# Performance work log

Hardware: AMD Instinct MI355X
Metric: run time of the kernel (lower is better)

The kernel has to match this reference:

```python
import jax, jax.numpy as jnp
import numpy as np

B_, H_, W_ = 4, 64, 64
D_MODEL, D_INNER, N_STATE, R_RANK, K_ = 96, 192, 16, 6, 4
EPS = 1e-5

def silu(v):
    return v * jax.nn.sigmoid(v)

def setup_inputs() -> dict:
    key = jax.random.key(0)
    ks = jax.random.split(key, 8)
    d, dm = D_INNER, D_MODEL
    A = jnp.tile(jnp.arange(1, N_STATE + 1, dtype=jnp.float32)[None, :], (K_ * d, 1))
    return {
        "x": jax.random.normal(ks[0], (B_, H_, W_, dm), jnp.float32),
        "in_proj_w": jax.random.normal(ks[1], (2 * d, dm), jnp.float32) * 0.02,
        "conv_w": jax.random.normal(ks[2], (d, 1, 3, 3), jnp.float32) * 0.1,
        "conv_b": jnp.zeros((d,), jnp.float32),
        "x_proj_weight": jax.random.normal(ks[3], (K_, R_RANK + 2 * N_STATE, d), jnp.float32) * 0.05,
        "dt_projs_weight": jax.random.normal(ks[4], (K_, d, R_RANK), jnp.float32) * 0.1,
        "dt_projs_bias": jax.random.normal(ks[5], (K_, d), jnp.float32) * 0.1,
        "A_logs": jnp.log(A),
        "Ds": jnp.ones((K_ * d,), jnp.float32),
        "out_norm_w": jnp.ones((d,), jnp.float32),
        "out_norm_b": jnp.zeros((d,), jnp.float32),
        "out_proj_w": jax.random.normal(ks[6], (dm, d), jnp.float32) * 0.02,
    }

def selective_scan(u, dts, As, Bs, Cs, Ds, dt_bias):
    # u, dts: [B,K,D,L]; As: [K,D,N]; Bs, Cs: [B,K,N,L]; Ds, dt_bias: [K,D]
    delta = jax.nn.softplus(dts + dt_bias[None, :, :, None])
    dT = jnp.moveaxis(delta, -1, 0)  # [L,B,K,D]
    uT = jnp.moveaxis(u, -1, 0)      # [L,B,K,D]
    BT = jnp.moveaxis(Bs, -1, 0)     # [L,B,K,N]
    CT = jnp.moveaxis(Cs, -1, 0)     # [L,B,K,N]
    h0 = jnp.zeros((u.shape[0], K_, D_INNER, N_STATE), jnp.float32)

    def step(h, inps):
        dt, ut, bt, ct = inps
        h = jnp.exp(dt[..., None] * As[None]) * h + (dt * ut)[..., None] * bt[:, :, None, :]
        y = jnp.einsum('bkdn,bkn->bkd', h, ct)
        return h, y

    _, ys = jax.lax.scan(step, h0, (dT, uT, BT, CT))
    ys = jnp.moveaxis(ys, 0, -1)  # [B,K,D,L]
    return ys + u * Ds[None, :, :, None]

def reference(x, in_proj_w, conv_w, conv_b, x_proj_weight, dt_projs_weight,
              dt_projs_bias, A_logs, Ds, out_norm_w, out_norm_b, out_proj_w):
    B, H, W, dm = x.shape
    d, N, R, K = D_INNER, N_STATE, R_RANK, K_
    L = H * W
    # in_proj + z gate (SiLU)
    xz = jnp.einsum('bhwc,pc->bhwp', x, in_proj_w)  # [B,H,W,2d]
    xc, z = xz[..., :d], xz[..., d:]
    z = silu(z)
    # depthwise conv (NCHW) + SiLU
    xc = jnp.transpose(xc, (0, 3, 1, 2))  # [B,d,H,W]
    xc = jax.lax.conv_general_dilated(
        xc, conv_w, (1, 1), 'SAME', feature_group_count=d,
        dimension_numbers=('NCHW', 'OIHW', 'NCHW')) + conv_b[None, :, None, None]
    xc = silu(xc)
    # cross-scan: 4 directions
    x0 = xc.reshape(B, d, L)                                   # row-major
    x1 = jnp.transpose(xc, (0, 1, 3, 2)).reshape(B, d, L)       # col-major
    xs = jnp.stack([x0, x1, x0[..., ::-1], x1[..., ::-1]], axis=1)  # [B,K,D,L]
    # projections
    x_dbl = jnp.einsum('bkdl,kcd->bkcl', xs, x_proj_weight)
    dts, Bs, Cs = jnp.split(x_dbl, [R, R + N], axis=2)
    dts = jnp.einsum('bkrl,kdr->bkdl', dts, dt_projs_weight)
    As = -jnp.exp(A_logs).reshape(K, d, N)
    ys = selective_scan(xs, dts, As, Bs, Cs, Ds.reshape(K, d), dt_projs_bias)
    # cross-merge
    y_wh = (ys[:, 1] + ys[:, 3, :, ::-1]).reshape(B, d, W, H)
    y_wh = jnp.transpose(y_wh, (0, 1, 3, 2)).reshape(B, d, L)
    y = ys[:, 0] + ys[:, 2, :, ::-1] + y_wh                     # [B,d,L]
    y = jnp.transpose(y.reshape(B, d, H, W), (0, 2, 3, 1))       # [B,H,W,d]
    # out_norm: LayerNorm over channel dim
    mu = jnp.mean(y, axis=-1, keepdims=True)
    var = jnp.mean((y - mu) ** 2, axis=-1, keepdims=True)
    y = out_norm_w * (y - mu) * jax.lax.rsqrt(var + EPS) + out_norm_b
    # gate + out_proj
    y = y * z
    return jnp.einsum('bhwd,cd->bhwc', y, out_proj_w)
```

## Files before the change

kernel.cpp:

```cpp
#include <hip/hip_runtime.h>
#include <math.h>

#define B_ 4
#define HH 64
#define WW 64
#define LL 4096
#define DM 96
#define DI 192
#define NS 16
#define RR 6
#define KK 4
#define NROW (B_ * KK * DI)
#define XPS 160
#define KOFF 40

__device__ __forceinline__ int pix_of(int k, int l) {
    switch (k) {
        case 0: return l;
        case 1: { int w = l >> 6, h = l & 63; return (h << 6) + w; }
        case 2: return (LL - 1) - l;
        default: { int ll = (LL - 1) - l; int w = ll >> 6, h = ll & 63; return (h << 6) + w; }
    }
}

__device__ __forceinline__ float silu_f(float v) {
    return v * __fdividef(1.f, 1.f + __expf(-v));
}
__device__ __forceinline__ float softplus_f(float x) {
    return (x > 20.f) ? x : __logf(1.f + __expf(x));
}

template<int MODE>
__global__ __launch_bounds__(256)
void gemm_kernel(const float* __restrict__ A, const float* __restrict__ Bw,
                 float* __restrict__ C0, float* __restrict__ C1,
                 int M, int N, int Kd) {
    __shared__ float As[32][68];
    __shared__ float Bs[32][68];
    int tid = threadIdx.x;
    int tx = tid & 15, ty = tid >> 4;
    int m0 = blockIdx.y * 64, n0 = blockIdx.x * 64;
    float acc[4][4] = {};
    for (int k0 = 0; k0 < Kd; k0 += 32) {
        #pragma unroll
        for (int i = 0; i < 8; ++i) {
            int idx = tid + i * 256;
            int r = idx >> 5, c = idx & 31;
            As[c][r] = A[(size_t)(m0 + r) * Kd + k0 + c];
            int rn = n0 + r;
            Bs[c][r] = (rn < N) ? Bw[(size_t)rn * Kd + k0 + c] : 0.f;
        }
        __syncthreads();
        #pragma unroll
        for (int kk = 0; kk < 32; ++kk) {
            float4 av = *(const float4*)&As[kk][ty * 4];
            float4 bv = *(const float4*)&Bs[kk][tx * 4];
            const float* avp = (const float*)&av;
            const float* bvp = (const float*)&bv;
            #pragma unroll
            for (int i = 0; i < 4; ++i)
                #pragma unroll
                for (int j = 0; j < 4; ++j)
                    acc[i][j] += avp[i] * bvp[j];
        }
        __syncthreads();
    }
    #pragma unroll
    for (int i = 0; i < 4; ++i) {
        int m = m0 + ty * 4 + i;
        #pragma unroll
        for (int j = 0; j < 4; ++j) {
            int n = n0 + tx * 4 + j;
            if (n >= N) continue;
            float v = acc[i][j];
            if (MODE == 0) {
                if (n < DI) C0[(size_t)m * DI + n] = v;
                else        C1[(size_t)m * DI + (n - DI)] = silu_f(v);
            } else if (MODE == 1) {
                C0[(size_t)m * N + n] = v;
            } else {
                if (n < 152) {
                    int kd = n / 38, c = n - kd * 38;
                    C0[(size_t)m * XPS + kd * KOFF + c] = v;
                }
            }
        }
    }
}

__global__ __launch_bounds__(192)
void conv_kernel(const float* __restrict__ xc, const float* __restrict__ cw,
                 const float* __restrict__ cb, float* __restrict__ out) {
    int p0 = blockIdx.x * 8;
    int b = blockIdx.y;
    int c = threadIdx.x;
    int h = p0 >> 6, w0 = p0 & 63;
    float kw[9];
    #pragma unroll
    for (int j = 0; j < 9; ++j) kw[j] = cw[c * 9 + j];
    float xv[3][10];
    #pragma unroll
    for (int dh = 0; dh < 3; ++dh) {
        int hh = h + dh - 1;
        bool hv = (hh >= 0 && hh < HH);
        #pragma unroll
        for (int j = 0; j < 10; ++j) {
            int ww = w0 + j - 1;
            bool v = hv && (ww >= 0 && ww < WW);
            xv[dh][j] = v ? xc[((size_t)(b << 12) + (hh << 6) + ww) * DI + c] : 0.f;
        }
    }
    float bias = cb[c];
    #pragma unroll
    for (int w = 0; w < 8; ++w) {
        float acc = bias;
        #pragma unroll
        for (int dh = 0; dh < 3; ++dh)
            #pragma unroll
            for (int dc = 0; dc < 3; ++dc)
                acc += xv[dh][w + dc] * kw[dh * 3 + dc];
        out[((size_t)(b << 12) + p0 + w) * DI + c] = silu_f(acc);
    }
}

__global__ __launch_bounds__(256)
void prep_kernel(const float* __restrict__ A_logs, int* __restrict__ flag) {
    int t = blockIdx.x * 256 + threadIdx.x;
    if (t >= KK * DI * NS) return;
    int n = t & 15;
    float an = -__expf(A_logs[t]);
    if (!(fabsf(an + (float)(n + 1)) < 1e-4f * (float)(n + 1))) atomicOr(flag, 1);
}

template<int PHASE, int NCHT>
__global__ __launch_bounds__(192)
void scan_phase(const float* __restrict__ xconv, const float* __restrict__ xdblP,
                const float* __restrict__ dtw, const float* __restrict__ dtb,
                const float* __restrict__ A_logs, const float* __restrict__ Ds,
                float* __restrict__ sumD, float* __restrict__ carryB,
                float* __restrict__ y_acc, const int* __restrict__ flag) {
    constexpr int CHL = LL / NCHT;
    constexpr int NV4 = (PHASE == 3) ? (KOFF / 4) : 6;
    int chunk = blockIdx.x;
    int k = blockIdx.y;
    int b = blockIdx.z;
    int d = threadIdx.x;
    int l0 = chunk * CHL;
    __shared__ float sx[CHL * NV4 * 4];
    float4* sx4 = (float4*)sx;
    const float* xb = xdblP + ((size_t)(b << 12)) * XPS + k * KOFF;
    for (int idx = d; idx < CHL * NV4; idx += DI) {
        int r = idx / NV4, j = idx - r * NV4;
        int p = pix_of(k, l0 + r);
        sx4[idx] = *(const float4*)(xb + (size_t)p * XPS + j * 4);
    }

    float wr[RR];
    #pragma unroll
    for (int r = 0; r < RR; ++r) wr[r] = dtw[(k * DI + d) * RR + r];
    float bias = dtb[k * DI + d];
    const float* alog = A_logs + (size_t)(k * DI + d) * NS;
    bool fastA = (*flag == 0);
    float h[NS];
    int row = (b * KK + k) * DI + d;
    if (PHASE == 1) {
        #pragma unroll
        for (int n = 0; n < NS; ++n) h[n] = 0.f;
    } else {
        const float4* cb4 = (const float4*)(carryB + ((size_t)chunk * NROW + row) * NS);
        #pragma unroll
        for (int q = 0; q < NS / 4; ++q) {
            float4 v = cb4[q];
            h[q * 4 + 0] = v.x; h[q * 4 + 1] = v.y;
            h[q * 4 + 2] = v.z; h[q * 4 + 3] = v.w;
        }
    }
    float Dk = (PHASE == 3) ? Ds[k * DI + d] : 0.f;
    float sumDelta = 0.f;
    __syncthreads();

    int s = (k == 0) ? 1 : (k == 1) ? 64 : (k == 2) ? -1 : -64;
    int p0 = pix_of(k, l0);
    intptr_t stp = (intptr_t)s * DI;
    const float* up = xconv + (size_t)(b << 12) * DI + (size_t)p0 * DI + d;
    float* yp = y_acc + (size_t)(b << 12) * DI + (size_t)p0 * DI + d;
    float u_cur = *up;

    for (int i = 0; i < CHL; ++i) {
        float u_nxt = 0.f;
        if (i + 1 < CHL) u_nxt = up[stp];
        float xrv[NV4 * 4];
        float4* x4 = (float4*)xrv;
        #pragma unroll
        for (int j = 0; j < NV4; ++j) x4[j] = sx4[i * NV4 + j];
        float dtraw = bias;
        #pragma unroll
        for (int r = 0; r < RR; ++r) dtraw += xrv[r] * wr[r];
        float delta = softplus_f(dtraw);
        if (PHASE == 1) sumDelta += delta;
        float du = delta * u_cur;
        float y = 0.f;
        if (fastA) {
            float g = __expf(-delta);
            float a = 1.f;
            #pragma unroll
            for (int n = 0; n < NS; ++n) {
                a *= g;
                h[n] = a * h[n] + du * xrv[6 + n];
                if (PHASE == 3) y += h[n] * xrv[22 + n];
            }
        } else {
            #pragma unroll
            for (int n = 0; n < NS; ++n) {
                float a = __expf(delta * (-__expf(alog[n])));
                h[n] = a * h[n] + du * xrv[6 + n];
                if (PHASE == 3) y += h[n] * xrv[22 + n];
            }
        }
        if (PHASE == 3) {
            y += u_cur * Dk;
            atomicAdd(yp, y);
            yp += stp;
        }
        up += stp;
        u_cur = u_nxt;
    }
    if (PHASE == 1) {
        float4* cb4 = (float4*)(carryB + ((size_t)chunk * NROW + row) * NS);
        #pragma unroll
        for (int q = 0; q < NS / 4; ++q) {
            float4 vb;
            vb.x = h[q * 4 + 0]; vb.y = h[q * 4 + 1];
            vb.z = h[q * 4 + 2]; vb.w = h[q * 4 + 3];
            cb4[q] = vb;
        }
        sumD[(size_t)chunk * NROW + row] = sumDelta;
    }
}

template<int NCHT>
__global__ __launch_bounds__(256)
void scan_chunks(const float* __restrict__ sumD, const float* __restrict__ A_logs,
                 float* __restrict__ carryB) {
    int t = blockIdx.x * 256 + threadIdx.x;
    if (t >= NROW * NS) return;
    int row = t >> 4, n = t & 15;
    int kd = row % (KK * DI);
    float An = -__expf(A_logs[(size_t)kd * NS + n]);
    float h = 0.f;
    for (int c = 0; c < NCHT; ++c) {
        size_t idx = (size_t)c * (NROW * NS) + t;
        float bb = carryB[idx];
        carryB[idx] = h;
        float a = __expf(An * sumD[(size_t)c * NROW + row]);
        h = a * h + bb;
    }
}

__global__ __launch_bounds__(256)
void ln_kernel(const float* __restrict__ y_acc, const float* __restrict__ z_silu,
               const float* __restrict__ nw, const float* __restrict__ nb,
               float* __restrict__ out) {
    int pg = blockIdx.x * 4 + (threadIdx.x >> 6);
    int lane = threadIdx.x & 63;
    const float* yr = y_acc + (size_t)pg * DI;
    float v0 = yr[lane], v1 = yr[lane + 64], v2 = yr[lane + 128];
    float s = v0 + v1 + v2;
    float sq = v0 * v0 + v1 * v1 + v2 * v2;
    #pragma unroll
    for (int m = 32; m >= 1; m >>= 1) {
        s  += __shfl_xor(s, m, 64);
        sq += __shfl_xor(sq, m, 64);
    }
    float mu = s * (1.f / 192.f);
    float var = sq * (1.f / 192.f) - mu * mu;
    float rs = rsqrtf(var + 1e-5f);
    const float* zr = z_silu + (size_t)pg * DI;
    float* o = out + (size_t)pg * DI;
    float vv[3] = {v0, v1, v2};
    #pragma unroll
    for (int j = 0; j < 3; ++j) {
        int c = lane + j * 64;
        o[c] = (nw[c] * (vv[j] - mu) * rs + nb[c]) * zr[c];
    }
}

extern "C" void kernel_launch(void* const* d_in, const int* in_sizes, int n_in,
                              void* d_out, int out_size, void* d_ws, size_t ws_size,
                              hipStream_t stream) {
    const float* x        = (const float*)d_in[0];
    const float* in_projw = (const float*)d_in[1];
    const float* conv_w   = (const float*)d_in[2];
    const float* conv_b   = (const float*)d_in[3];
    const float* x_projw  = (const float*)d_in[4];
    const float* dt_w     = (const float*)d_in[5];
    const float* dt_b     = (const float*)d_in[6];
    const float* A_logs   = (const float*)d_in[7];
    const float* Ds       = (const float*)d_in[8];
    const float* nw       = (const float*)d_in[9];
    const float* nb       = (const float*)d_in[10];
    const float* opw      = (const float*)d_in[11];
    float* out = (float*)d_out;
    float* ws = (float*)d_ws;

    const size_t SZ = (size_t)B_ * LL * DI;
    const size_t XD = (size_t)B_ * LL * XPS;
    const size_t CAR256 = (size_t)NROW * 256 * NS;
    const size_t CAR128 = (size_t)NROW * 128 * NS;
    const size_t need256 = (3 * SZ + XD + CAR256 + (size_t)NROW * 256 + 16) * sizeof(float);
    bool big = (ws_size >= need256);

    float* z_silu = ws;
    float* xc_raw = ws + SZ;
    float* xconv  = ws + 2 * SZ;
    float* xdblP  = ws + 3 * SZ;
    float* carryB = ws + 3 * SZ + XD;
    float* sumD   = carryB + (big ? CAR256 : CAR128);
    int*   flag   = (int*)(sumD + (size_t)NROW * (big ? 256 : 128));
    float* y_acc  = xc_raw;
    float* yln    = xconv;

    gemm_kernel<0><<<dim3(6, 256), 256, 0, stream>>>(x, in_projw, xc_raw, z_silu,
                                                     B_ * LL, 2 * DI, DM);
    hipMemsetAsync(flag, 0, sizeof(int), stream);
    prep_kernel<<<(KK * DI * NS + 255) / 256, 256, 0, stream>>>(A_logs, flag);
    conv_kernel<<<dim3(LL / 8, B_), DI, 0, stream>>>(xc_raw, conv_w, conv_b, xconv);
    gemm_kernel<2><<<dim3(3, 256), 256, 0, stream>>>(xconv, x_projw, xdblP, nullptr,
                                                     B_ * LL, 152, DI);

    if (big) {
        scan_phase<1, 256><<<dim3(256, KK, B_), DI, 0, stream>>>(xconv, xdblP, dt_w, dt_b,
                                                                 A_logs, Ds, sumD, carryB, nullptr, flag);
        scan_chunks<256><<<(NROW * NS + 255) / 256, 256, 0, stream>>>(sumD, A_logs, carryB);
        hipMemsetAsync(y_acc, 0, SZ * sizeof(float), stream);
        scan_phase<3, 256><<<dim3(256, KK, B_), DI, 0, stream>>>(xconv, xdblP, dt_w, dt_b,
                                                                 A_logs, Ds, sumD, carryB, y_acc, flag);
    } else {
        scan_phase<1, 128><<<dim3(128, KK, B_), DI, 0, stream>>>(xconv, xdblP, dt_w, dt_b,
                                                                 A_logs, Ds, sumD, carryB, nullptr, flag);
        scan_chunks<128><<<(NROW * NS + 255) / 256, 256, 0, stream>>>(sumD, A_logs, carryB);
        hipMemsetAsync(y_acc, 0, SZ * sizeof(float), stream);
        scan_phase<3, 128><<<dim3(128, KK, B_), DI, 0, stream>>>(xconv, xdblP, dt_w, dt_b,
                                                                 A_logs, Ds, sumD, carryB, y_acc, flag);
    }
    ln_kernel<<<(B_ * LL) / 4, 256, 0, stream>>>(y_acc, z_silu, nw, nb, yln);
    gemm_kernel<1><<<dim3(2, 256), 256, 0, stream>>>(yln, opw, out, nullptr,
                                                     B_ * LL, DM, DI);
}
```

Measured before the change: 235.0 us.

## Pair forward/reverse scan directions per block and drop atomic y accumulation

Each scan block now processes a direction and its reversed counterpart (k and k+2) over mirrored chunks, so both touch the same pixels. Outputs go into a shared-memory accumulator and are written once with plain stores. Results land in two buffers (row-pair and column-pair) that the LayerNorm kernel sums, which removes the global atomics and the y memset. The cost is an extra workspace buffer and two sequential phase-3 launches with fewer blocks each. The xdbl rows are now read straight from global memory instead of being staged in LDS.

Measured after the change: 257.6 us. 9.6% more time.

```diff
diff --git a/kernel.cpp b/kernel.cpp
--- a/kernel.cpp
+++ b/kernel.cpp
@@ -134,71 +134,72 @@
 
 template<int PHASE, int NCHT>
 __global__ __launch_bounds__(192)
-void scan_phase(const float* __restrict__ xconv, const float* __restrict__ xdblP,
-                const float* __restrict__ dtw, const float* __restrict__ dtb,
-                const float* __restrict__ A_logs, const float* __restrict__ Ds,
-                float* __restrict__ sumD, float* __restrict__ carryB,
-                float* __restrict__ y_acc, const int* __restrict__ flag) {
+void scan_paired(const float* __restrict__ xconv, const float* __restrict__ xdblP,
+                 const float* __restrict__ dtw, const float* __restrict__ dtb,
+                 const float* __restrict__ A_logs, const float* __restrict__ Ds,
+                 float* __restrict__ sumD, float* __restrict__ carryB,
+                 float* __restrict__ yout, const int* __restrict__ flag, int pairArg) {
     constexpr int CHL = LL / NCHT;
     constexpr int NV4 = (PHASE == 3) ? (KOFF / 4) : 6;
-    int chunk = blockIdx.x;
-    int k = blockIdx.y;
+    int c = blockIdx.x;
+    int pair = (PHASE == 1) ? blockIdx.y : pairArg;
     int b = blockIdx.z;
     int d = threadIdx.x;
-    int l0 = chunk * CHL;
-    __shared__ float sx[CHL * NV4 * 4];
-    float4* sx4 = (float4*)sx;
-    const float* xb = xdblP + ((size_t)(b << 12)) * XPS + k * KOFF;
-    for (int idx = d; idx < CHL * NV4; idx += DI) {
-        int r = idx / NV4, j = idx - r * NV4;
-        int p = pix_of(k, l0 + r);
-        sx4[idx] = *(const float4*)(xb + (size_t)p * XPS + j * 4);
-    }
-
-    float wr[RR];
-    #pragma unroll
-    for (int r = 0; r < RR; ++r) wr[r] = dtw[(k * DI + d) * RR + r];
-    float bias = dtb[k * DI + d];
-    const float* alog = A_logs + (size_t)(k * DI + d) * NS;
+    int k0 = pair, k1 = pair + 2;
+    int c2 = NCHT - 1 - c;
+    int s = (pair == 0) ? 1 : 64;
+    int p0 = pix_of(k0, c * CHL);
+    __shared__ float sy[(PHASE == 3) ? (CHL * DI) : 4];
+
+    if (PHASE == 3) {
+        for (int idx = d; idx < CHL * DI; idx += DI) sy[idx] = 0.f;
+    }
+
+    float wr0[RR], wr1[RR];
+    #pragma unroll
+    for (int r = 0; r < RR; ++r) {
+        wr0[r] = dtw[(k0 * DI + d) * RR + r];
+        wr1[r] = dtw[(k1 * DI + d) * RR + r];
+    }
+    float bias0 = dtb[k0 * DI + d], bias1 = dtb[k1 * DI + d];
+    const float* alog0 = A_logs + (size_t)(k0 * DI + d) * NS;
+    const float* alog1 = A_logs + (size_t)(k1 * DI + d) * NS;
     bool fastA = (*flag == 0);
-    float h[NS];
-    int row = (b * KK + k) * DI + d;
+    int row0 = (b * KK + k0) * DI + d;
+    int row1 = (b * KK + k1) * DI + d;
+    float h0[NS], h1[NS];
     if (PHASE == 1) {
         #pragma unroll
-        for (int n = 0; n < NS; ++n) h[n] = 0.f;
+        for (int n = 0; n < NS; ++n) { h0[n] = 0.f; h1[n] = 0.f; }
     } else {
-        const float4* cb4 = (const float4*)(carryB + ((size_t)chunk * NROW + row) * NS);
+        const float4* ca = (const float4*)(carryB + ((size_t)c * NROW + row0) * NS);
+        const float4* cb = (const float4*)(carryB + ((size_t)c2 * NROW + row1) * NS);
         #pragma unroll
         for (int q = 0; q < NS / 4; ++q) {
-            float4 v = cb4[q];
-            h[q * 4 + 0] = v.x; h[q * 4 + 1] = v.y;
-            h[q * 4 + 2] = v.z; h[q * 4 + 3] = v.w;
-        }
-    }
-    float Dk = (PHASE == 3) ? Ds[k * DI + d] : 0.f;
-    float sumDelta = 0.f;
-    __syncthreads();
-
-    int s = (k == 0) ? 1 : (k == 1) ? 64 : (k == 2) ? -1 : -64;
-    int p0 = pix_of(k, l0);
-    intptr_t stp = (intptr_t)s * DI;
-    const float* up = xconv + (size_t)(b << 12) * DI + (size_t)p0 * DI + d;
-    float* yp = y_acc + (size_t)(b << 12) * DI + (size_t)p0 * DI + d;
-    float u_cur = *up;
-
-    for (int i = 0; i < CHL; ++i) {
-        float u_nxt = 0.f;
-        if (i + 1 < CHL) u_nxt = up[stp];
+            float4 va = ca[q], vb = cb[q];
+            h0[q * 4 + 0] = va.x; h0[q * 4 + 1] = va.y; h0[q * 4 + 2] = va.z; h0[q * 4 + 3] = va.w;
+            h1[q * 4 + 0] = vb.x; h1[q * 4 + 1] = vb.y; h1[q * 4 + 2] = vb.z; h1[q * 4 + 3] = vb.w;
+        }
+    }
+    float Dk0 = (PHASE == 3) ? Ds[k0 * DI + d] : 0.f;
+    float Dk1 = (PHASE == 3) ? Ds[k1 * DI + d] : 0.f;
+    float sum0 = 0.f, sum1 = 0.f;
+    const float* ub = xconv + ((size_t)(b << 12) + p0) * DI + d;
+    const float* xrow = xdblP + ((size_t)(b << 12) + p0) * XPS;
+    intptr_t xstp = (intptr_t)s * XPS;
+    intptr_t ustp = (intptr_t)s * DI;
+
+    auto dstep = [&](const float* __restrict__ xr, float u, const float* wr, float biasv,
+                     const float* alog, float Dkv, float* h, float& sd) -> float {
         float xrv[NV4 * 4];
-        float4* x4 = (float4*)xrv;
-        #pragma unroll
-        for (int j = 0; j < NV4; ++j) x4[j] = sx4[i * NV4 + j];
-        float dtraw = bias;
+        #pragma unroll
+        for (int j = 0; j < NV4; ++j) ((float4*)xrv)[j] = ((const float4*)xr)[j];
+        float dtraw = biasv;
         #pragma unroll
         for (int r = 0; r < RR; ++r) dtraw += xrv[r] * wr[r];
         float delta = softplus_f(dtraw);
-        if (PHASE == 1) sumDelta += delta;
-        float du = delta * u_cur;
+        if (PHASE == 1) sd += delta;
+        float du = delta * u;
         float y = 0.f;
         if (fastA) {
             float g = __expf(-delta);
@@ -217,24 +218,37 @@
                 if (PHASE == 3) y += h[n] * xrv[22 + n];
             }
         }
+        if (PHASE == 3) y += u * Dkv;
+        return y;
+    };
+
+    for (int i = 0; i < CHL; ++i) {
+        int ri = CHL - 1 - i;
+        float u0 = ub[(intptr_t)i * ustp];
+        float u1 = ub[(intptr_t)ri * ustp];
+        float y0 = dstep(xrow + (intptr_t)i * xstp + k0 * KOFF, u0, wr0, bias0, alog0, Dk0, h0, sum0);
+        float y1 = dstep(xrow + (intptr_t)ri * xstp + k1 * KOFF, u1, wr1, bias1, alog1, Dk1, h1, sum1);
         if (PHASE == 3) {
-            y += u_cur * Dk;
-            atomicAdd(yp, y);
-            yp += stp;
-        }
-        up += stp;
-        u_cur = u_nxt;
-    }
-    if (PHASE == 1) {
-        float4* cb4 = (float4*)(carryB + ((size_t)chunk * NROW + row) * NS);
+            sy[i * DI + d] += y0;
+            sy[ri * DI + d] += y1;
+        }
+    }
+
+    if (PHASE == 3) {
+        float* yo = yout + ((size_t)(b << 12) + p0) * DI + d;
+        for (int r = 0; r < CHL; ++r) yo[(intptr_t)r * ustp] = sy[r * DI + d];
+    } else {
+        float4* ca = (float4*)(carryB + ((size_t)c * NROW + row0) * NS);
+        float4* cb = (float4*)(carryB + ((size_t)c2 * NROW + row1) * NS);
         #pragma unroll
         for (int q = 0; q < NS / 4; ++q) {
-            float4 vb;
-            vb.x = h[q * 4 + 0]; vb.y = h[q * 4 + 1];
-            vb.z = h[q * 4 + 2]; vb.w = h[q * 4 + 3];
-            cb4[q] = vb;
-        }
-        sumD[(size_t)chunk * NROW + row] = sumDelta;
+            float4 va, vb;
+            va.x = h0[q * 4 + 0]; va.y = h0[q * 4 + 1]; va.z = h0[q * 4 + 2]; va.w = h0[q * 4 + 3];
+            vb.x = h1[q * 4 + 0]; vb.y = h1[q * 4 + 1]; vb.z = h1[q * 4 + 2]; vb.w = h1[q * 4 + 3];
+            ca[q] = va; cb[q] = vb;
+        }
+        sumD[(size_t)c * NROW + row0] = sum0;
+        sumD[(size_t)c2 * NROW + row1] = sum1;
     }
 }
 
@@ -248,6 +262,7 @@
     int kd = row % (KK * DI);
     float An = -__expf(A_logs[(size_t)kd * NS + n]);
     float h = 0.f;
+    #pragma unroll 4
     for (int c = 0; c < NCHT; ++c) {
         size_t idx = (size_t)c * (NROW * NS) + t;
         float bb = carryB[idx];
@@ -258,13 +273,17 @@
 }
 
 __global__ __launch_bounds__(256)
-void ln_kernel(const float* __restrict__ y_acc, const float* __restrict__ z_silu,
+void ln_kernel(const float* __restrict__ yA, const float* __restrict__ yB,
+               const float* __restrict__ z_silu,
                const float* __restrict__ nw, const float* __restrict__ nb,
                float* __restrict__ out) {
     int pg = blockIdx.x * 4 + (threadIdx.x >> 6);
     int lane = threadIdx.x & 63;
-    const float* yr = y_acc + (size_t)pg * DI;
-    float v0 = yr[lane], v1 = yr[lane + 64], v2 = yr[lane + 128];
+    const float* ya = yA + (size_t)pg * DI;
+    const float* yb = yB + (size_t)pg * DI;
+    float v0 = ya[lane] + yb[lane];
+    float v1 = ya[lane + 64] + yb[lane + 64];
+    float v2 = ya[lane + 128] + yb[lane + 128];
     float s = v0 + v1 + v2;
     float sq = v0 * v0 + v1 * v1 + v2 * v2;
     #pragma unroll
@@ -307,17 +326,20 @@
     const size_t XD = (size_t)B_ * LL * XPS;
     const size_t CAR256 = (size_t)NROW * 256 * NS;
     const size_t CAR128 = (size_t)NROW * 128 * NS;
-    const size_t need256 = (3 * SZ + XD + CAR256 + (size_t)NROW * 256 + 16) * sizeof(float);
+    const size_t need256 = (4 * SZ + XD + CAR256 + (size_t)NROW * 256 + 16) * sizeof(float);
     bool big = (ws_size >= need256);
+    const size_t CAR = big ? CAR256 : CAR128;
+    const int NCH = big ? 256 : 128;
 
     float* z_silu = ws;
-    float* xc_raw = ws + SZ;
+    float* yA     = ws + SZ;
     float* xconv  = ws + 2 * SZ;
-    float* xdblP  = ws + 3 * SZ;
-    float* carryB = ws + 3 * SZ + XD;
-    float* sumD   = carryB + (big ? CAR256 : CAR128);
-    int*   flag   = (int*)(sumD + (size_t)NROW * (big ? 256 : 128));
-    float* y_acc  = xc_raw;
+    float* yB     = ws + 3 * SZ;
+    float* xdblP  = ws + 4 * SZ;
+    float* carryB = ws + 4 * SZ + XD;
+    float* sumD   = carryB + CAR;
+    int*   flag   = (int*)(sumD + (size_t)NROW * NCH);
+    float* xc_raw = yA;
     float* yln    = xconv;
 
     gemm_kernel<0><<<dim3(6, 256), 256, 0, stream>>>(x, in_projw, xc_raw, z_silu,
@@ -329,21 +351,23 @@
                                                      B_ * LL, 152, DI);
 
     if (big) {
-        scan_phase<1, 256><<<dim3(256, KK, B_), DI, 0, stream>>>(xconv, xdblP, dt_w, dt_b,
-                                                                 A_logs, Ds, sumD, carryB, nullptr, flag);
+        scan_paired<1, 256><<<dim3(256, 2, B_), 192, 0, stream>>>(xconv, xdblP, dt_w, dt_b,
+                                                                  A_logs, Ds, sumD, carryB, nullptr, flag, 0);
         scan_chunks<256><<<(NROW * NS + 255) / 256, 256, 0, stream>>>(sumD, A_logs, carryB);
-        hipMemsetAsync(y_acc, 0, SZ * sizeof(float), stream);
-        scan_phase<3, 256><<<dim3(256, KK, B_), DI, 0, stream>>>(xconv, xdblP, dt_w, dt_b,
-                                                                 A_logs, Ds, sumD, carryB, y_acc, flag);
+        scan_paired<3, 256><<<dim3(256, 1, B_), 192, 0, stream>>>(xconv, xdblP, dt_w, dt_b,
+                                                                  A_logs, Ds, sumD, carryB, yA, flag, 0);
+        scan_paired<3, 256><<<dim3(256, 1, B_), 192, 0, stream>>>(xconv, xdblP, dt_w, dt_b,
+                                                                  A_logs, Ds, sumD, carryB, yB, flag, 1);
     } else {
-        scan_phase<1, 128><<<dim3(128, KK, B_), DI, 0, stream>>>(xconv, xdblP, dt_w, dt_b,
-                                                                 A_logs, Ds, sumD, carryB, nullptr, flag);
+        scan_paired<1, 128><<<dim3(128, 2, B_), 192, 0, stream>>>(xconv, xdblP, dt_w, dt_b,
+                                                                  A_logs, Ds, sumD, carryB, nullptr, flag, 0);
         scan_chunks<128><<<(NROW * NS + 255) / 256, 256, 0, stream>>>(sumD, A_logs, carryB);
-        hipMemsetAsync(y_acc, 0, SZ * sizeof(float), stream);
-        scan_phase<3, 128><<<dim3(128, KK, B_), DI, 0, stream>>>(xconv, xdblP, dt_w, dt_b,
-                                                                 A_logs, Ds, sumD, carryB, y_acc, flag);
-    }
-    ln_kernel<<<(B_ * LL) / 4, 256, 0, stream>>>(y_acc, z_silu, nw, nb, yln);
+        scan_paired<3, 128><<<dim3(128, 1, B_), 192, 0, stream>>>(xconv, xdblP, dt_w, dt_b,
+                                                                  A_logs, Ds, sumD, carryB, yA, flag, 0);
+        scan_paired<3, 128><<<dim3(128, 1, B_), 192, 0, stream>>>(xconv, xdblP, dt_w, dt_b,
+                                                                  A_logs, Ds, sumD, carryB, yB, flag, 1);
+    }
+    ln_kernel<<<(B_ * LL) / 4, 256, 0, stream>>>(yA, yB, z_silu, nw, nb, yln);
     gemm_kernel<1><<<dim3(2, 256), 256, 0, stream>>>(yln, opw, out, nullptr,
                                                      B_ * LL, DM, DI);
 }
```
